# Optimization experiments

Measured on AMD Instinct MI355X. Metric: run time of the kernel, lower is better.

The kernel has to match this reference:

```python
import jax, jax.numpy as jnp
import numpy as np

B, N, M = 2, 8192, 8192
PEN_RATIO = 0.95
REG_W = 0.001
LOSS_W = 1.0
EPS_COS = 1e-8


def quat_to_rot(q):
    # q: [..., 4] in (x, y, z, w) order (legacy kornia convention), assumed normalized
    x, y, z, w = q[..., 0], q[..., 1], q[..., 2], q[..., 3]
    r0 = jnp.stack([1 - 2 * (y * y + z * z), 2 * (x * y - z * w), 2 * (x * z + y * w)], -1)
    r1 = jnp.stack([2 * (x * y + z * w), 1 - 2 * (x * x + z * z), 2 * (y * z - x * w)], -1)
    r2 = jnp.stack([2 * (x * z - y * w), 2 * (y * z + x * w), 1 - 2 * (x * x + y * y)], -1)
    return jnp.stack([r0, r1, r2], -2)


def span_cov(cp):
    # cp: [N,7] -> SPD cov [N,3,3]; eigenvalues are cumulative sums (e0, e0+e1, e0+e1+e2)
    e0 = cp[:, 0]
    e1 = e0 + cp[:, 1]
    e2 = e1 + cp[:, 2]
    eig = jnp.stack([e0, e1, e2], -1)  # [N,3]
    q = cp[:, 3:] / (jnp.linalg.norm(cp[:, 3:], axis=-1, keepdims=True) + 1e-9)
    E = quat_to_rot(q)  # [N,3,3]
    return jnp.einsum('nij,nj,nkj->nik', E, eig, E)


def setup_inputs() -> dict:
    key = jax.random.key(0)
    ks = jax.random.split(key, 8)
    return {
        'xyz_pred': jax.random.normal(ks[0], (B, N, 3), jnp.float32) * 10.0,
        'xyz_target': jax.random.normal(ks[1], (B, M, 3), jnp.float32) * 10.0,
        'cov_pred': jax.random.uniform(ks[2], (B, N, 7), jnp.float32),
        'cov_target': jax.random.uniform(ks[3], (B, M, 7), jnp.float32),
        'R_pred': jax.random.normal(ks[4], (B, 3, 3), jnp.float32),
        't_pred': jax.random.normal(ks[5], (B, 3), jnp.float32),
        'normal_pred': jax.random.normal(ks[6], (B, N, 3), jnp.float32),
        'normal_target': jax.random.normal(ks[7], (B, M, 3), jnp.float32),
    }


def reference(xyz_pred, xyz_target, cov_pred, cov_target, R_pred, t_pred, normal_pred, normal_target):
    def per_batch(xp, xt, cp, ct, R, nrm):
        covp = span_cov(cp)  # [N,3,3]
        covt = span_cov(ct)  # [M,3,3]
        # one-direction chamfer: squared NN distance + index (||p||^2+||t||^2-2 p.t)
        d2 = (xp * xp).sum(-1)[:, None] + (xt * xt).sum(-1)[None, :] - 2.0 * (xp @ xt.T)  # [N,M]
        diff = d2.min(axis=1)          # [N]
        idx = jnp.argmin(d2, axis=1)   # [N]
        xa = xt[idx]                   # associated target points
        cpa = covt[idx]                # associated target covariances
        dv = xp - xa
        # ROI mask via kth value: k = 1 + int(N*ratio) (1-indexed) -> sorted[int(N*ratio)]
        m = jnp.maximum(jnp.sort(diff)[int(N * PEN_RATIO)], 1.0)
        cm = (diff < m).astype(xp.dtype)
        nvalid = cm.sum()
        Rd = jax.lax.stop_gradient(R)
        sigma = covp + jnp.einsum('ij,njk,lk->nil', Rd, cpa, Rd)
        sigma_inv = jnp.linalg.inv(sigma)
        sq = jnp.einsum('ni,nij,nj->n', dv, sigma_inv, dv)  # Mahalanobis sq dist
        logdet = jnp.log(jnp.linalg.det(sigma))
        loss_b = (sq * cm).sum() / nvalid + REG_W * (0.5 * logdet * cm).sum() / nvalid
        # weighted SVD registration head (single ICP iter), all detached as in torch
        diff_na = xa - xp
        cossim = (nrm * diff_na).sum(-1) / jnp.maximum(
            jnp.linalg.norm(nrm, axis=-1) * jnp.linalg.norm(diff_na, axis=-1), EPS_COS)
        w = jax.lax.stop_gradient(jnp.abs(cossim) ** 2 * cm)
        src = jax.lax.stop_gradient(xp)
        tgt = jax.lax.stop_gradient(xa)
        wn = w / w.sum()
        sc = (wn[:, None] * src).sum(0)
        tc = (wn[:, None] * tgt).sum(0)
        H = jnp.einsum('n,ni,nj->ij', w, src - sc, tgt - tc)
        U, S, Vt = jnp.linalg.svd(H)
        V = Vt.T
        d = jnp.linalg.det(V @ U.T)
        Rres = V @ jnp.diag(jnp.stack([jnp.ones_like(d), jnp.ones_like(d), d])) @ U.T
        tres = tc - Rres @ sc
        return loss_b, Rres, tres

    losses, Rs, ts = jax.vmap(per_batch)(xyz_pred, xyz_target, cov_pred, cov_target, R_pred, normal_pred)
    return LOSS_W * losses.sum(), Rs, ts
```

## Files before the change

kernel.cpp:

```cpp
#include <hip/hip_runtime.h>
#include <math.h>

#define B_ 2
#define N_ 8192
#define M_ 8192
#define KSEL 7782
#define CH 128
#define CHS (M_ / CH)
#define PTS 1024
#define PPT 4

__device__ __forceinline__ unsigned ord_of(float f) {
  unsigned u = __float_as_uint(f);
  return (u & 0x80000000u) ? ~u : (u | 0x80000000u);
}
__device__ __forceinline__ float float_of_ord(unsigned o) {
  unsigned u = (o & 0x80000000u) ? (o ^ 0x80000000u) : ~o;
  return __uint_as_float(u);
}

__global__ __launch_bounds__(256) void init_kernel(
    unsigned long long* __restrict__ keys, const float* __restrict__ xt,
    float* __restrict__ tnorm) {
  const int gid = blockIdx.x * 256 + threadIdx.x;
  keys[gid] = 0xFFFFFFFFFFFFFFFFull;
  float tx = xt[gid * 3 + 0], ty = xt[gid * 3 + 1], tz = xt[gid * 3 + 2];
  tnorm[gid] = tx * tx + ty * ty + tz * tz;
}

__global__ __launch_bounds__(256, 8) void nn_kernel(
    const float* __restrict__ xp, const float* __restrict__ xt,
    const float* __restrict__ tnorm, unsigned long long* __restrict__ keys) {
  const int b = blockIdx.z;
  const int pblk = blockIdx.x;
  const int ch = blockIdx.y;

  __shared__ float4 tg[CHS];
  const float* __restrict__ xtb = xt + ((size_t)b * M_ + (size_t)ch * CHS) * 3;
  const float* __restrict__ twb = tnorm + (size_t)b * M_ + (size_t)ch * CHS;
  if (threadIdx.x < CHS) {
    const int j = threadIdx.x;
    tg[j] = make_float4(xtb[3 * j + 0], xtb[3 * j + 1], xtb[3 * j + 2],
                        twb[j]);
  }
  __syncthreads();

  const int i0 = pblk * PTS + threadIdx.x;
  float xm[PPT], ym[PPT], zm[PPT], nrm2[PPT], best[PPT];
  int bi[PPT];
#pragma unroll
  for (int k = 0; k < PPT; ++k) {
    const float* p = xp + ((size_t)b * N_ + i0 + k * 256) * 3;
    float x = p[0], y = p[1], z = p[2];
    nrm2[k] = x * x + y * y + z * z;
    xm[k] = -2.0f * x;
    ym[k] = -2.0f * y;
    zm[k] = -2.0f * z;
    best[k] = 3.4e38f;
    bi[k] = 0;
  }

#pragma unroll 2
  for (int j = 0; j < CHS; ++j) {
    float4 t = tg[j];
#pragma unroll
    for (int k = 0; k < PPT; ++k) {
      float d = fmaf(t.x, xm[k], fmaf(t.y, ym[k], fmaf(t.z, zm[k], t.w)));
      if (d < best[k]) { best[k] = d; bi[k] = j; }
    }
  }

  const int base = ch * CHS;
#pragma unroll
  for (int k = 0; k < PPT; ++k) {
    unsigned long long key =
        ((unsigned long long)ord_of(best[k] + nrm2[k]) << 32) |
        (unsigned)(base + bi[k]);
    atomicMin(&keys[(size_t)b * N_ + i0 + k * 256], key);
  }
}

__global__ __launch_bounds__(1024) void sel_kernel(
    const unsigned long long* __restrict__ keys, float* __restrict__ mout,
    double* __restrict__ acc) {
  __shared__ unsigned hist[256];
  __shared__ unsigned sel_digit, sel_rank;
  const int b = blockIdx.x;

  if (threadIdx.x < 32) acc[b * 32 + threadIdx.x] = 0.0;

  unsigned v[8];
#pragma unroll
  for (int t = 0; t < 8; ++t)
    v[t] = (unsigned)(keys[(size_t)b * N_ + threadIdx.x + t * 1024] >> 32);

  unsigned prefix = 0;
  unsigned rank = KSEL;

#pragma unroll
  for (int pass = 0; pass < 4; ++pass) {
    const int shift = 24 - pass * 8;
    const unsigned pmask = (pass == 0) ? 0u : (0xFFFFFFFFu << (shift + 8));

    if (threadIdx.x < 256) hist[threadIdx.x] = 0;
    __syncthreads();

#pragma unroll
    for (int t = 0; t < 8; ++t) {
      if ((v[t] & pmask) == prefix)
        atomicAdd(&hist[(v[t] >> shift) & 0xFFu], 1u);
    }
    __syncthreads();

    if (threadIdx.x < 64) {
      const int lane = threadIdx.x;
      unsigned h0 = hist[lane * 4 + 0], h1 = hist[lane * 4 + 1];
      unsigned h2 = hist[lane * 4 + 2], h3 = hist[lane * 4 + 3];
      unsigned c0 = h0, c1 = c0 + h1, c2 = c1 + h2, c3 = c2 + h3;
      unsigned s = c3;
#pragma unroll
      for (int off = 1; off < 64; off <<= 1) {
        unsigned t = __shfl_up(s, off);
        if (lane >= off) s += t;
      }
      unsigned excl = s - c3;
      unsigned r = rank;
      if (r >= excl && r < excl + c0) { sel_digit = lane * 4 + 0; sel_rank = r - excl; }
      if (r >= excl + c0 && r < excl + c1) { sel_digit = lane * 4 + 1; sel_rank = r - (excl + c0); }
      if (r >= excl + c1 && r < excl + c2) { sel_digit = lane * 4 + 2; sel_rank = r - (excl + c1); }
      if (r >= excl + c2 && r < excl + c3) { sel_digit = lane * 4 + 3; sel_rank = r - (excl + c2); }
    }
    __syncthreads();
    prefix |= (sel_digit << shift);
    rank = sel_rank;
    __syncthreads();
  }

  if (threadIdx.x == 0) {
    float f = float_of_ord(prefix);
    mout[b] = fmaxf(f, 1.0f);
  }
}

__device__ __forceinline__ void cov_from_params(const float* __restrict__ c,
                                                float C[3][3]) {
  float e0 = c[0];
  float e1 = e0 + c[1];
  float e2 = e1 + c[2];
  float qx = c[3], qy = c[4], qz = c[5], qw = c[6];
  float qn = sqrtf(qx * qx + qy * qy + qz * qz + qw * qw) + 1e-9f;
  float x = qx / qn, y = qy / qn, z = qz / qn, w = qw / qn;
  float E[3][3];
  E[0][0] = 1.0f - 2.0f * (y * y + z * z);
  E[0][1] = 2.0f * (x * y - z * w);
  E[0][2] = 2.0f * (x * z + y * w);
  E[1][0] = 2.0f * (x * y + z * w);
  E[1][1] = 1.0f - 2.0f * (x * x + z * z);
  E[1][2] = 2.0f * (y * z - x * w);
  E[2][0] = 2.0f * (x * z - y * w);
  E[2][1] = 2.0f * (y * z + x * w);
  E[2][2] = 1.0f - 2.0f * (x * x + y * y);
#pragma unroll
  for (int i = 0; i < 3; ++i)
#pragma unroll
    for (int k = 0; k < 3; ++k)
      C[i][k] = e0 * E[i][0] * E[k][0] + e1 * E[i][1] * E[k][1] +
                e2 * E[i][2] * E[k][2];
}

__global__ __launch_bounds__(256) void main_kernel(
    const float* __restrict__ xp, const float* __restrict__ xt,
    const float* __restrict__ cpp, const float* __restrict__ ctp,
    const float* __restrict__ Rp, const float* __restrict__ nrm,
    const unsigned long long* __restrict__ keys, const float* __restrict__ mout,
    double* __restrict__ acc) {
  const int b = blockIdx.y;
  const int i = blockIdx.x * 256 + threadIdx.x;

  float R[3][3];
#pragma unroll
  for (int r = 0; r < 3; ++r)
#pragma unroll
    for (int c = 0; c < 3; ++c) R[r][c] = Rp[b * 9 + r * 3 + c];
  const float m = mout[b];

  unsigned long long key = keys[(size_t)b * N_ + i];
  float d2 = float_of_ord((unsigned)(key >> 32));
  int id = (int)(key & 0xFFFFFFFFull);

  const float* p = xp + ((size_t)b * N_ + i) * 3;
  float px = p[0], py = p[1], pz = p[2];
  const float* a_ = xt + ((size_t)b * M_ + id) * 3;
  float ax = a_[0], ay = a_[1], az = a_[2];

  float cmv = (d2 < m) ? 1.0f : 0.0f;

  float Cp[3][3], Ct[3][3];
  cov_from_params(cpp + ((size_t)b * N_ + i) * 7, Cp);
  cov_from_params(ctp + ((size_t)b * M_ + id) * 7, Ct);

  float T[3][3], G[3][3];
#pragma unroll
  for (int r = 0; r < 3; ++r)
#pragma unroll
    for (int c = 0; c < 3; ++c)
      T[r][c] = R[r][0] * Ct[0][c] + R[r][1] * Ct[1][c] + R[r][2] * Ct[2][c];
#pragma unroll
  for (int r = 0; r < 3; ++r)
#pragma unroll
    for (int c = 0; c < 3; ++c)
      G[r][c] = Cp[r][c] +
                (T[r][0] * R[c][0] + T[r][1] * R[c][1] + T[r][2] * R[c][2]);

  float c00 = G[1][1] * G[2][2] - G[1][2] * G[2][1];
  float c01 = G[1][2] * G[2][0] - G[1][0] * G[2][2];
  float c02 = G[1][0] * G[2][1] - G[1][1] * G[2][0];
  float det = G[0][0] * c00 + G[0][1] * c01 + G[0][2] * c02;
  float rdet = 1.0f / det;
  float i00 = (G[1][1] * G[2][2] - G[1][2] * G[2][1]) * rdet;
  float i01 = (G[0][2] * G[2][1] - G[0][1] * G[2][2]) * rdet;
  float i02 = (G[0][1] * G[1][2] - G[0][2] * G[1][1]) * rdet;
  float i10 = (G[1][2] * G[2][0] - G[1][0] * G[2][2]) * rdet;
  float i11 = (G[0][0] * G[2][2] - G[0][2] * G[2][0]) * rdet;
  float i12 = (G[0][2] * G[1][0] - G[0][0] * G[1][2]) * rdet;
  float i20 = (G[1][0] * G[2][1] - G[1][1] * G[2][0]) * rdet;
  float i21 = (G[0][1] * G[2][0] - G[0][0] * G[2][1]) * rdet;
  float i22 = (G[0][0] * G[1][1] - G[0][1] * G[1][0]) * rdet;

  float dvx = px - ax, dvy = py - ay, dvz = pz - az;
  float t0 = i00 * dvx + i01 * dvy + i02 * dvz;
  float t1 = i10 * dvx + i11 * dvy + i12 * dvz;
  float t2 = i20 * dvx + i21 * dvy + i22 * dvz;
  float sq = dvx * t0 + dvy * t1 + dvz * t2;
  float logdet = logf(det);

  const float* nv = nrm + ((size_t)b * N_ + i) * 3;
  float nx = nv[0], ny = nv[1], nz = nv[2];
  float gx = ax - px, gy = ay - py, gz = az - pz;
  float dt = nx * gx + ny * gy + nz * gz;
  float den = fmaxf(sqrtf(nx * nx + ny * ny + nz * nz) *
                        sqrtf(gx * gx + gy * gy + gz * gz),
                    1e-8f);
  float cs = dt / den;
  float w = cs * cs * cmv;

  __shared__ double red[4][19];
  const int lane = threadIdx.x & 63, wv = threadIdx.x >> 6;

#define REDUCE_ONE(expr, kidx)                          \
  {                                                     \
    double v_ = (expr);                                 \
    v_ += __shfl_down(v_, 32);                          \
    v_ += __shfl_down(v_, 16);                          \
    v_ += __shfl_down(v_, 8);                           \
    v_ += __shfl_down(v_, 4);                           \
    v_ += __shfl_down(v_, 2);                           \
    v_ += __shfl_down(v_, 1);                           \
    if (lane == 0) red[wv][kidx] = v_;                  \
  }

  REDUCE_ONE((double)cmv, 0)
  REDUCE_ONE((double)sq * (double)cmv, 1)
  REDUCE_ONE((double)logdet * (double)cmv, 2)
  REDUCE_ONE((double)w, 3)
  REDUCE_ONE((double)w * px, 4)
  REDUCE_ONE((double)w * py, 5)
  REDUCE_ONE((double)w * pz, 6)
  REDUCE_ONE((double)w * ax, 7)
  REDUCE_ONE((double)w * ay, 8)
  REDUCE_ONE((double)w * az, 9)
  REDUCE_ONE((double)w * (double)px * (double)ax, 10)
  REDUCE_ONE((double)w * (double)px * (double)ay, 11)
  REDUCE_ONE((double)w * (double)px * (double)az, 12)
  REDUCE_ONE((double)w * (double)py * (double)ax, 13)
  REDUCE_ONE((double)w * (double)py * (double)ay, 14)
  REDUCE_ONE((double)w * (double)py * (double)az, 15)
  REDUCE_ONE((double)w * (double)pz * (double)ax, 16)
  REDUCE_ONE((double)w * (double)pz * (double)ay, 17)
  REDUCE_ONE((double)w * (double)pz * (double)az, 18)
#undef REDUCE_ONE

  __syncthreads();
  if (threadIdx.x < 19) {
    double s = red[0][threadIdx.x] + red[1][threadIdx.x] +
               red[2][threadIdx.x] + red[3][threadIdx.x];
    atomicAdd(&acc[b * 32 + threadIdx.x], s);
  }
}

__device__ float det3f(const float M[3][3]) {
  return M[0][0] * (M[1][1] * M[2][2] - M[1][2] * M[2][1]) -
         M[0][1] * (M[1][0] * M[2][2] - M[1][2] * M[2][0]) +
         M[0][2] * (M[1][0] * M[2][1] - M[1][1] * M[2][0]);
}

__device__ __forceinline__ void eigvec3f(const float A[3][3], float lam,
                                         float& vx, float& vy, float& vz) {
  float r00 = A[0][0] - lam, r01 = A[0][1], r02 = A[0][2];
  float r10 = A[0][1], r11 = A[1][1] - lam, r12 = A[1][2];
  float r20 = A[0][2], r21 = A[1][2], r22 = A[2][2] - lam;

  float ax = r01 * r12 - r02 * r11;
  float ay = r02 * r10 - r00 * r12;
  float az = r00 * r11 - r01 * r10;
  float bx = r01 * r22 - r02 * r21;
  float by = r02 * r20 - r00 * r22;
  float bz = r00 * r21 - r01 * r20;
  float cx = r11 * r22 - r12 * r21;
  float cy = r12 * r20 - r10 * r22;
  float cz = r10 * r21 - r11 * r20;

  float na = ax * ax + ay * ay + az * az;
  float nb = bx * bx + by * by + bz * bz;
  float nc = cx * cx + cy * cy + cz * cz;

  bool pickB = nb > na;
  float sx = pickB ? bx : ax, sy = pickB ? by : ay, sz = pickB ? bz : az;
  float sn = pickB ? nb : na;
  bool pickC = nc > sn;
  sx = pickC ? cx : sx; sy = pickC ? cy : sy; sz = pickC ? cz : sz;
  sn = pickC ? nc : sn;

  float inv = (sn > 0.0f) ? 1.0f / sqrtf(sn) : 0.0f;
  vx = sx * inv;
  vy = sy * inv;
  vz = sz * inv;
  if (inv == 0.0f) vx = 1.0f;
}

__device__ void kabschf(const float H[3][3], float R[3][3]) {
  float A[3][3];
#pragma unroll
  for (int i = 0; i < 3; ++i)
#pragma unroll
    for (int j = 0; j < 3; ++j)
      A[i][j] = H[0][i] * H[0][j] + H[1][i] * H[1][j] + H[2][i] * H[2][j];

  float lam0, lam1, lam2;
  float v0x, v0y, v0z, v1x, v1y, v1z, v2x, v2y, v2z;

  float mtr = (A[0][0] + A[1][1] + A[2][2]) / 3.0f;
  float K00 = A[0][0] - mtr, K11 = A[1][1] - mtr, K22 = A[2][2] - mtr;
  float a01 = A[0][1], a02 = A[0][2], a12 = A[1][2];
  float p2 = K00 * K00 + K11 * K11 + K22 * K22 +
             2.0f * (a01 * a01 + a02 * a02 + a12 * a12);
  float p = sqrtf(p2 / 6.0f);
  if (p < 1e-12f) {
    lam0 = lam1 = lam2 = mtr;
    v0x = 1.0f; v0y = 0.0f; v0z = 0.0f;
    v1x = 0.0f; v1y = 1.0f; v1z = 0.0f;
    v2x = 0.0f; v2y = 0.0f; v2z = 1.0f;
  } else {
    float detK = K00 * (K11 * K22 - a12 * a12) -
                 a01 * (a01 * K22 - a12 * a02) +
                 a02 * (a01 * a12 - K11 * a02);
    float rr = detK / (2.0f * p * p * p);
    rr = fminf(1.0f, fmaxf(-1.0f, rr));
    float phi = acosf(rr) / 3.0f;
    lam0 = mtr + 2.0f * p * cosf(phi);
    lam2 = mtr + 2.0f * p * cosf(phi + 2.0943951023931953f);
    lam1 = 3.0f * mtr - lam0 - lam2;

    eigvec3f(A, lam0, v0x, v0y, v0z);
    eigvec3f(A, lam1, v1x, v1y, v1z);
    float dp = v1x * v0x + v1y * v0y + v1z * v0z;
    v1x -= dp * v0x;
    v1y -= dp * v0y;
    v1z -= dp * v0z;
    float n1 = v1x * v1x + v1y * v1y + v1z * v1z;
    if (n1 > 1e-20f) {
      float inv = 1.0f / sqrtf(n1);
      v1x *= inv; v1y *= inv; v1z *= inv;
    } else {
      float fx = fabsf(v0x), fy = fabsf(v0y), fz = fabsf(v0z);
      bool xMin = (fx <= fy) && (fx <= fz);
      bool yMin = !xMin && (fy <= fz);
      float tx = xMin ? 1.0f : 0.0f;
      float ty = yMin ? 1.0f : 0.0f;
      float tz = (!xMin && !yMin) ? 1.0f : 0.0f;
      v1x = v0y * tz - v0z * ty;
      v1y = v0z * tx - v0x * tz;
      v1z = v0x * ty - v0y * tx;
      float inv = 1.0f / sqrtf(v1x * v1x + v1y * v1y + v1z * v1z);
      v1x *= inv; v1y *= inv; v1z *= inv;
    }
    v2x = v0y * v1z - v0z * v1y;
    v2y = v0z * v1x - v0x * v1z;
    v2z = v0x * v1y - v0y * v1x;
  }

  float Vs[3][3];
  Vs[0][0] = v0x; Vs[1][0] = v0y; Vs[2][0] = v0z;
  Vs[0][1] = v1x; Vs[1][1] = v1y; Vs[2][1] = v1z;
  Vs[0][2] = v2x; Vs[1][2] = v2y; Vs[2][2] = v2z;

  float sg0 = sqrtf(fmaxf(lam0, 0.0f));
  float sg1 = sqrtf(fmaxf(lam1, 0.0f));
  float sg2 = sqrtf(fmaxf(lam2, 0.0f));

  float U[3][3];
  {
    float sg[3] = {sg0, sg1, sg2};
#pragma unroll
    for (int c = 0; c < 3; ++c) {
      float ux = H[0][0] * Vs[0][c] + H[0][1] * Vs[1][c] + H[0][2] * Vs[2][c];
      float uy = H[1][0] * Vs[0][c] + H[1][1] * Vs[1][c] + H[1][2] * Vs[2][c];
      float uz = H[2][0] * Vs[0][c] + H[2][1] * Vs[1][c] + H[2][2] * Vs[2][c];
      float inv = (sg[c] > 1e-6f * sg0 + 1e-30f) ? 1.0f / sg[c] : 0.0f;
      U[0][c] = ux * inv;
      U[1][c] = uy * inv;
      U[2][c] = uz * inv;
    }
  }
  if (sg2 <= 1e-6f * sg0 + 1e-30f) {
    U[0][2] = U[1][0] * U[2][1] - U[2][0] * U[1][1];
    U[1][2] = U[2][0] * U[0][1] - U[0][0] * U[2][1];
    U[2][2] = U[0][0] * U[1][1] - U[1][0] * U[0][1];
  }
  float d = det3f(U) * det3f(Vs);
#pragma unroll
  for (int i = 0; i < 3; ++i)
#pragma unroll
    for (int j = 0; j < 3; ++j)
      R[i][j] = Vs[i][0] * U[j][0] + Vs[i][1] * U[j][1] + d * Vs[i][2] * U[j][2];
}

__global__ __launch_bounds__(64) void finalize_kernel(
    const double* __restrict__ acc, float* __restrict__ out) {
  __shared__ double lossb[B_];
  const int b = threadIdx.x;
  if (b < B_) {
    const double* a = acc + b * 32;
    double cnt = a[0], ssq = a[1], sld = a[2], W = a[3];
    double loss = ssq / cnt + 0.001 * 0.5 * sld / cnt;
    lossb[b] = loss;
    double Ss[3] = {a[4], a[5], a[6]}, St[3] = {a[7], a[8], a[9]};
    double sc[3], tc[3];
#pragma unroll
    for (int c = 0; c < 3; ++c) { sc[c] = Ss[c] / W; tc[c] = St[c] / W; }
    double H[3][3];
    double hmax = 1e-30;
#pragma unroll
    for (int r = 0; r < 3; ++r)
#pragma unroll
      for (int c = 0; c < 3; ++c) {
        H[r][c] = a[10 + r * 3 + c] - Ss[r] * St[c] / W;
        double ab = fabs(H[r][c]);
        if (ab > hmax) hmax = ab;
      }
    float Hf[3][3];
    double rinv = 1.0 / hmax;
#pragma unroll
    for (int r = 0; r < 3; ++r)
#pragma unroll
      for (int c = 0; c < 3; ++c) Hf[r][c] = (float)(H[r][c] * rinv);
    float Rf[3][3];
    kabschf(Hf, Rf);
#pragma unroll
    for (int r = 0; r < 3; ++r)
#pragma unroll
      for (int c = 0; c < 3; ++c)
        out[1 + b * 9 + r * 3 + c] = Rf[r][c];
#pragma unroll
    for (int r = 0; r < 3; ++r) {
      double t = tc[r] - ((double)Rf[r][0] * sc[0] + (double)Rf[r][1] * sc[1] +
                          (double)Rf[r][2] * sc[2]);
      out[1 + B_ * 9 + b * 3 + r] = (float)t;
    }
  }
  __syncthreads();
  if (threadIdx.x == 0) out[0] = (float)(lossb[0] + lossb[1]);
}

extern "C" void kernel_launch(void* const* d_in, const int* in_sizes, int n_in,
                              void* d_out, int out_size, void* d_ws,
                              size_t ws_size, hipStream_t stream) {
  const float* xyz_pred = (const float*)d_in[0];
  const float* xyz_target = (const float*)d_in[1];
  const float* cov_pred = (const float*)d_in[2];
  const float* cov_target = (const float*)d_in[3];
  const float* R_pred = (const float*)d_in[4];
  const float* normal_pred = (const float*)d_in[6];
  float* out = (float*)d_out;

  char* ws = (char*)d_ws;
  double* acc = (double*)ws;
  unsigned long long* keys = (unsigned long long*)(ws + 512);
  float* mout = (float*)(ws + 512 + (size_t)B_ * N_ * 8);
  float* tnorm = (float*)(ws + 1024 + (size_t)B_ * N_ * 8);

  hipLaunchKernelGGL(init_kernel, dim3(B_ * M_ / 256), dim3(256), 0, stream,
                     keys, xyz_target, tnorm);
  hipLaunchKernelGGL(nn_kernel, dim3(N_ / PTS, CH, B_), dim3(256), 0, stream,
                     xyz_pred, xyz_target, tnorm, keys);
  hipLaunchKernelGGL(sel_kernel, dim3(B_), dim3(1024), 0, stream, keys, mout,
                     acc);
  hipLaunchKernelGGL(main_kernel, dim3(N_ / 256, B_), dim3(256), 0, stream,
                     xyz_pred, xyz_target, cov_pred, cov_target, R_pred,
                     normal_pred, keys, mout, acc);
  hipLaunchKernelGGL(finalize_kernel, dim3(1), dim3(64), 0, stream, acc, out);
}
```

Baseline: 48.05 us.

## Fuse radix select, main loss and finalize into one tail kernel

Merges the selection, per-point loss and finalize kernels into a single tail kernel. Each block redundantly recomputes the batch's radix-select threshold, and the last block to finish (found through an atomic counter) runs the Kabsch finalize. Accumulator zeroing moves into the init kernel. This removes two kernel launches and their inter-kernel gaps. In exchange, all 32 blocks per batch repeat the 8192-key histogram passes with only 256 threads each.

```diff
diff --git a/kernel.cpp b/kernel.cpp
--- a/kernel.cpp
+++ b/kernel.cpp
@@ -21,11 +21,14 @@
 
 __global__ __launch_bounds__(256) void init_kernel(
     unsigned long long* __restrict__ keys, const float* __restrict__ xt,
-    float* __restrict__ tnorm) {
+    float* __restrict__ tnorm, double* __restrict__ acc,
+    unsigned* __restrict__ done) {
   const int gid = blockIdx.x * 256 + threadIdx.x;
   keys[gid] = 0xFFFFFFFFFFFFFFFFull;
   float tx = xt[gid * 3 + 0], ty = xt[gid * 3 + 1], tz = xt[gid * 3 + 2];
   tnorm[gid] = tx * tx + ty * ty + tz * tz;
+  if (gid < B_ * 32) acc[gid] = 0.0;
+  if (gid == 0) *done = 0u;
 }
 
 __global__ __launch_bounds__(256, 8) void nn_kernel(
@@ -77,68 +80,6 @@
         ((unsigned long long)ord_of(best[k] + nrm2[k]) << 32) |
         (unsigned)(base + bi[k]);
     atomicMin(&keys[(size_t)b * N_ + i0 + k * 256], key);
-  }
-}
-
-__global__ __launch_bounds__(1024) void sel_kernel(
-    const unsigned long long* __restrict__ keys, float* __restrict__ mout,
-    double* __restrict__ acc) {
-  __shared__ unsigned hist[256];
-  __shared__ unsigned sel_digit, sel_rank;
-  const int b = blockIdx.x;
-
-  if (threadIdx.x < 32) acc[b * 32 + threadIdx.x] = 0.0;
-
-  unsigned v[8];
-#pragma unroll
-  for (int t = 0; t < 8; ++t)
-    v[t] = (unsigned)(keys[(size_t)b * N_ + threadIdx.x + t * 1024] >> 32);
-
-  unsigned prefix = 0;
-  unsigned rank = KSEL;
-
-#pragma unroll
-  for (int pass = 0; pass < 4; ++pass) {
-    const int shift = 24 - pass * 8;
-    const unsigned pmask = (pass == 0) ? 0u : (0xFFFFFFFFu << (shift + 8));
-
-    if (threadIdx.x < 256) hist[threadIdx.x] = 0;
-    __syncthreads();
-
-#pragma unroll
-    for (int t = 0; t < 8; ++t) {
-      if ((v[t] & pmask) == prefix)
-        atomicAdd(&hist[(v[t] >> shift) & 0xFFu], 1u);
-    }
-    __syncthreads();
-
-    if (threadIdx.x < 64) {
-      const int lane = threadIdx.x;
-      unsigned h0 = hist[lane * 4 + 0], h1 = hist[lane * 4 + 1];
-      unsigned h2 = hist[lane * 4 + 2], h3 = hist[lane * 4 + 3];
-      unsigned c0 = h0, c1 = c0 + h1, c2 = c1 + h2, c3 = c2 + h3;
-      unsigned s = c3;
-#pragma unroll
-      for (int off = 1; off < 64; off <<= 1) {
-        unsigned t = __shfl_up(s, off);
-        if (lane >= off) s += t;
-      }
-      unsigned excl = s - c3;
-      unsigned r = rank;
-      if (r >= excl && r < excl + c0) { sel_digit = lane * 4 + 0; sel_rank = r - excl; }
-      if (r >= excl + c0 && r < excl + c1) { sel_digit = lane * 4 + 1; sel_rank = r - (excl + c0); }
-      if (r >= excl + c1 && r < excl + c2) { sel_digit = lane * 4 + 2; sel_rank = r - (excl + c1); }
-      if (r >= excl + c2 && r < excl + c3) { sel_digit = lane * 4 + 3; sel_rank = r - (excl + c2); }
-    }
-    __syncthreads();
-    prefix |= (sel_digit << shift);
-    rank = sel_rank;
-    __syncthreads();
-  }
-
-  if (threadIdx.x == 0) {
-    float f = float_of_ord(prefix);
-    mout[b] = fmaxf(f, 1.0f);
   }
 }
 
@@ -166,126 +107,6 @@
     for (int k = 0; k < 3; ++k)
       C[i][k] = e0 * E[i][0] * E[k][0] + e1 * E[i][1] * E[k][1] +
                 e2 * E[i][2] * E[k][2];
-}
-
-__global__ __launch_bounds__(256) void main_kernel(
-    const float* __restrict__ xp, const float* __restrict__ xt,
-    const float* __restrict__ cpp, const float* __restrict__ ctp,
-    const float* __restrict__ Rp, const float* __restrict__ nrm,
-    const unsigned long long* __restrict__ keys, const float* __restrict__ mout,
-    double* __restrict__ acc) {
-  const int b = blockIdx.y;
-  const int i = blockIdx.x * 256 + threadIdx.x;
-
-  float R[3][3];
-#pragma unroll
-  for (int r = 0; r < 3; ++r)
-#pragma unroll
-    for (int c = 0; c < 3; ++c) R[r][c] = Rp[b * 9 + r * 3 + c];
-  const float m = mout[b];
-
-  unsigned long long key = keys[(size_t)b * N_ + i];
-  float d2 = float_of_ord((unsigned)(key >> 32));
-  int id = (int)(key & 0xFFFFFFFFull);
-
-  const float* p = xp + ((size_t)b * N_ + i) * 3;
-  float px = p[0], py = p[1], pz = p[2];
-  const float* a_ = xt + ((size_t)b * M_ + id) * 3;
-  float ax = a_[0], ay = a_[1], az = a_[2];
-
-  float cmv = (d2 < m) ? 1.0f : 0.0f;
-
-  float Cp[3][3], Ct[3][3];
-  cov_from_params(cpp + ((size_t)b * N_ + i) * 7, Cp);
-  cov_from_params(ctp + ((size_t)b * M_ + id) * 7, Ct);
-
-  float T[3][3], G[3][3];
-#pragma unroll
-  for (int r = 0; r < 3; ++r)
-#pragma unroll
-    for (int c = 0; c < 3; ++c)
-      T[r][c] = R[r][0] * Ct[0][c] + R[r][1] * Ct[1][c] + R[r][2] * Ct[2][c];
-#pragma unroll
-  for (int r = 0; r < 3; ++r)
-#pragma unroll
-    for (int c = 0; c < 3; ++c)
-      G[r][c] = Cp[r][c] +
-                (T[r][0] * R[c][0] + T[r][1] * R[c][1] + T[r][2] * R[c][2]);
-
-  float c00 = G[1][1] * G[2][2] - G[1][2] * G[2][1];
-  float c01 = G[1][2] * G[2][0] - G[1][0] * G[2][2];
-  float c02 = G[1][0] * G[2][1] - G[1][1] * G[2][0];
-  float det = G[0][0] * c00 + G[0][1] * c01 + G[0][2] * c02;
-  float rdet = 1.0f / det;
-  float i00 = (G[1][1] * G[2][2] - G[1][2] * G[2][1]) * rdet;
-  float i01 = (G[0][2] * G[2][1] - G[0][1] * G[2][2]) * rdet;
-  float i02 = (G[0][1] * G[1][2] - G[0][2] * G[1][1]) * rdet;
-  float i10 = (G[1][2] * G[2][0] - G[1][0] * G[2][2]) * rdet;
-  float i11 = (G[0][0] * G[2][2] - G[0][2] * G[2][0]) * rdet;
-  float i12 = (G[0][2] * G[1][0] - G[0][0] * G[1][2]) * rdet;
-  float i20 = (G[1][0] * G[2][1] - G[1][1] * G[2][0]) * rdet;
-  float i21 = (G[0][1] * G[2][0] - G[0][0] * G[2][1]) * rdet;
-  float i22 = (G[0][0] * G[1][1] - G[0][1] * G[1][0]) * rdet;
-
-  float dvx = px - ax, dvy = py - ay, dvz = pz - az;
-  float t0 = i00 * dvx + i01 * dvy + i02 * dvz;
-  float t1 = i10 * dvx + i11 * dvy + i12 * dvz;
-  float t2 = i20 * dvx + i21 * dvy + i22 * dvz;
-  float sq = dvx * t0 + dvy * t1 + dvz * t2;
-  float logdet = logf(det);
-
-  const float* nv = nrm + ((size_t)b * N_ + i) * 3;
-  float nx = nv[0], ny = nv[1], nz = nv[2];
-  float gx = ax - px, gy = ay - py, gz = az - pz;
-  float dt = nx * gx + ny * gy + nz * gz;
-  float den = fmaxf(sqrtf(nx * nx + ny * ny + nz * nz) *
-                        sqrtf(gx * gx + gy * gy + gz * gz),
-                    1e-8f);
-  float cs = dt / den;
-  float w = cs * cs * cmv;
-
-  __shared__ double red[4][19];
-  const int lane = threadIdx.x & 63, wv = threadIdx.x >> 6;
-
-#define REDUCE_ONE(expr, kidx)                          \
-  {                                                     \
-    double v_ = (expr);                                 \
-    v_ += __shfl_down(v_, 32);                          \
-    v_ += __shfl_down(v_, 16);                          \
-    v_ += __shfl_down(v_, 8);                           \
-    v_ += __shfl_down(v_, 4);                           \
-    v_ += __shfl_down(v_, 2);                           \
-    v_ += __shfl_down(v_, 1);                           \
-    if (lane == 0) red[wv][kidx] = v_;                  \
-  }
-
-  REDUCE_ONE((double)cmv, 0)
-  REDUCE_ONE((double)sq * (double)cmv, 1)
-  REDUCE_ONE((double)logdet * (double)cmv, 2)
-  REDUCE_ONE((double)w, 3)
-  REDUCE_ONE((double)w * px, 4)
-  REDUCE_ONE((double)w * py, 5)
-  REDUCE_ONE((double)w * pz, 6)
-  REDUCE_ONE((double)w * ax, 7)
-  REDUCE_ONE((double)w * ay, 8)
-  REDUCE_ONE((double)w * az, 9)
-  REDUCE_ONE((double)w * (double)px * (double)ax, 10)
-  REDUCE_ONE((double)w * (double)px * (double)ay, 11)
-  REDUCE_ONE((double)w * (double)px * (double)az, 12)
-  REDUCE_ONE((double)w * (double)py * (double)ax, 13)
-  REDUCE_ONE((double)w * (double)py * (double)ay, 14)
-  REDUCE_ONE((double)w * (double)py * (double)az, 15)
-  REDUCE_ONE((double)w * (double)pz * (double)ax, 16)
-  REDUCE_ONE((double)w * (double)pz * (double)ay, 17)
-  REDUCE_ONE((double)w * (double)pz * (double)az, 18)
-#undef REDUCE_ONE
-
-  __syncthreads();
-  if (threadIdx.x < 19) {
-    double s = red[0][threadIdx.x] + red[1][threadIdx.x] +
-               red[2][threadIdx.x] + red[3][threadIdx.x];
-    atomicAdd(&acc[b * 32 + threadIdx.x], s);
-  }
 }
 
 __device__ float det3f(const float M[3][3]) {
@@ -425,15 +246,192 @@
       R[i][j] = Vs[i][0] * U[j][0] + Vs[i][1] * U[j][1] + d * Vs[i][2] * U[j][2];
 }
 
-__global__ __launch_bounds__(64) void finalize_kernel(
-    const double* __restrict__ acc, float* __restrict__ out) {
+__global__ __launch_bounds__(256) void tail_kernel(
+    const float* __restrict__ xp, const float* __restrict__ xt,
+    const float* __restrict__ cpp, const float* __restrict__ ctp,
+    const float* __restrict__ Rp, const float* __restrict__ nrm,
+    const unsigned long long* __restrict__ keys, double* __restrict__ acc,
+    unsigned* __restrict__ done, float* __restrict__ out) {
+  const int b = blockIdx.y;
+  const unsigned* __restrict__ keyhi =
+      (const unsigned*)(keys + (size_t)b * N_) + 1;
+
+  __shared__ unsigned hist[256];
+  __shared__ unsigned sel_digit, sel_rank;
+  __shared__ float m_sh;
+  {
+    unsigned prefix = 0, rank = KSEL;
+#pragma unroll
+    for (int pass = 0; pass < 4; ++pass) {
+      const int shift = 24 - pass * 8;
+      const unsigned pmask = (pass == 0) ? 0u : (0xFFFFFFFFu << (shift + 8));
+      hist[threadIdx.x] = 0;
+      __syncthreads();
+#pragma unroll 4
+      for (int t = 0; t < 32; ++t) {
+        unsigned v = keyhi[2 * (threadIdx.x + t * 256)];
+        if ((v & pmask) == prefix)
+          atomicAdd(&hist[(v >> shift) & 0xFFu], 1u);
+      }
+      __syncthreads();
+      if (threadIdx.x < 64) {
+        const int lane = threadIdx.x;
+        unsigned h0 = hist[lane * 4 + 0], h1 = hist[lane * 4 + 1];
+        unsigned h2 = hist[lane * 4 + 2], h3 = hist[lane * 4 + 3];
+        unsigned c0 = h0, c1 = c0 + h1, c2 = c1 + h2, c3 = c2 + h3;
+        unsigned s = c3;
+#pragma unroll
+        for (int off = 1; off < 64; off <<= 1) {
+          unsigned t = __shfl_up(s, off);
+          if (lane >= off) s += t;
+        }
+        unsigned excl = s - c3;
+        unsigned r = rank;
+        if (r >= excl && r < excl + c0) { sel_digit = lane * 4 + 0; sel_rank = r - excl; }
+        if (r >= excl + c0 && r < excl + c1) { sel_digit = lane * 4 + 1; sel_rank = r - (excl + c0); }
+        if (r >= excl + c1 && r < excl + c2) { sel_digit = lane * 4 + 2; sel_rank = r - (excl + c1); }
+        if (r >= excl + c2 && r < excl + c3) { sel_digit = lane * 4 + 3; sel_rank = r - (excl + c2); }
+      }
+      __syncthreads();
+      prefix |= (sel_digit << shift);
+      rank = sel_rank;
+      __syncthreads();
+    }
+    if (threadIdx.x == 0) m_sh = fmaxf(float_of_ord(prefix), 1.0f);
+    __syncthreads();
+  }
+  const float m = m_sh;
+
+  const int i = blockIdx.x * 256 + threadIdx.x;
+
+  float R[3][3];
+#pragma unroll
+  for (int r = 0; r < 3; ++r)
+#pragma unroll
+    for (int c = 0; c < 3; ++c) R[r][c] = Rp[b * 9 + r * 3 + c];
+
+  unsigned long long key = keys[(size_t)b * N_ + i];
+  float d2 = float_of_ord((unsigned)(key >> 32));
+  int id = (int)(key & 0xFFFFFFFFull);
+
+  const float* p = xp + ((size_t)b * N_ + i) * 3;
+  float px = p[0], py = p[1], pz = p[2];
+  const float* a_ = xt + ((size_t)b * M_ + id) * 3;
+  float ax = a_[0], ay = a_[1], az = a_[2];
+
+  float cmv = (d2 < m) ? 1.0f : 0.0f;
+
+  float Cp[3][3], Ct[3][3];
+  cov_from_params(cpp + ((size_t)b * N_ + i) * 7, Cp);
+  cov_from_params(ctp + ((size_t)b * M_ + id) * 7, Ct);
+
+  float T[3][3], G[3][3];
+#pragma unroll
+  for (int r = 0; r < 3; ++r)
+#pragma unroll
+    for (int c = 0; c < 3; ++c)
+      T[r][c] = R[r][0] * Ct[0][c] + R[r][1] * Ct[1][c] + R[r][2] * Ct[2][c];
+#pragma unroll
+  for (int r = 0; r < 3; ++r)
+#pragma unroll
+    for (int c = 0; c < 3; ++c)
+      G[r][c] = Cp[r][c] +
+                (T[r][0] * R[c][0] + T[r][1] * R[c][1] + T[r][2] * R[c][2]);
+
+  float c00 = G[1][1] * G[2][2] - G[1][2] * G[2][1];
+  float c01 = G[1][2] * G[2][0] - G[1][0] * G[2][2];
+  float c02 = G[1][0] * G[2][1] - G[1][1] * G[2][0];
+  float det = G[0][0] * c00 + G[0][1] * c01 + G[0][2] * c02;
+  float rdet = 1.0f / det;
+  float i00 = (G[1][1] * G[2][2] - G[1][2] * G[2][1]) * rdet;
+  float i01 = (G[0][2] * G[2][1] - G[0][1] * G[2][2]) * rdet;
+  float i02 = (G[0][1] * G[1][2] - G[0][2] * G[1][1]) * rdet;
+  float i10 = (G[1][2] * G[2][0] - G[1][0] * G[2][2]) * rdet;
+  float i11 = (G[0][0] * G[2][2] - G[0][2] * G[2][0]) * rdet;
+  float i12 = (G[0][2] * G[1][0] - G[0][0] * G[1][2]) * rdet;
+  float i20 = (G[1][0] * G[2][1] - G[1][1] * G[2][0]) * rdet;
+  float i21 = (G[0][1] * G[2][0] - G[0][0] * G[2][1]) * rdet;
+  float i22 = (G[0][0] * G[1][1] - G[0][1] * G[1][0]) * rdet;
+
+  float dvx = px - ax, dvy = py - ay, dvz = pz - az;
+  float t0 = i00 * dvx + i01 * dvy + i02 * dvz;
+  float t1 = i10 * dvx + i11 * dvy + i12 * dvz;
+  float t2 = i20 * dvx + i21 * dvy + i22 * dvz;
+  float sq = dvx * t0 + dvy * t1 + dvz * t2;
+  float logdet = logf(det);
+
+  const float* nv = nrm + ((size_t)b * N_ + i) * 3;
+  float nx = nv[0], ny = nv[1], nz = nv[2];
+  float gx = ax - px, gy = ay - py, gz = az - pz;
+  float dt = nx * gx + ny * gy + nz * gz;
+  float den = fmaxf(sqrtf(nx * nx + ny * ny + nz * nz) *
+                        sqrtf(gx * gx + gy * gy + gz * gz),
+                    1e-8f);
+  float cs = dt / den;
+  float w = cs * cs * cmv;
+
+  __shared__ double red[4][19];
+  const int lane = threadIdx.x & 63, wv = threadIdx.x >> 6;
+
+#define REDUCE_ONE(expr, kidx)                          \
+  {                                                     \
+    double v_ = (expr);                                 \
+    v_ += __shfl_down(v_, 32);                          \
+    v_ += __shfl_down(v_, 16);                          \
+    v_ += __shfl_down(v_, 8);                           \
+    v_ += __shfl_down(v_, 4);                           \
+    v_ += __shfl_down(v_, 2);                           \
+    v_ += __shfl_down(v_, 1);                           \
+    if (lane == 0) red[wv][kidx] = v_;                  \
+  }
+
+  REDUCE_ONE((double)cmv, 0)
+  REDUCE_ONE((double)sq * (double)cmv, 1)
+  REDUCE_ONE((double)logdet * (double)cmv, 2)
+  REDUCE_ONE((double)w, 3)
+  REDUCE_ONE((double)w * px, 4)
+  REDUCE_ONE((double)w * py, 5)
+  REDUCE_ONE((double)w * pz, 6)
+  REDUCE_ONE((double)w * ax, 7)
+  REDUCE_ONE((double)w * ay, 8)
+  REDUCE_ONE((double)w * az, 9)
+  REDUCE_ONE((double)w * (double)px * (double)ax, 10)
+  REDUCE_ONE((double)w * (double)px * (double)ay, 11)
+  REDUCE_ONE((double)w * (double)px * (double)az, 12)
+  REDUCE_ONE((double)w * (double)py * (double)ax, 13)
+  REDUCE_ONE((double)w * (double)py * (double)ay, 14)
+  REDUCE_ONE((double)w * (double)py * (double)az, 15)
+  REDUCE_ONE((double)w * (double)pz * (double)ax, 16)
+  REDUCE_ONE((double)w * (double)pz * (double)ay, 17)
+  REDUCE_ONE((double)w * (double)pz * (double)az, 18)
+#undef REDUCE_ONE
+
+  __syncthreads();
+  if (threadIdx.x < 19) {
+    double s = red[0][threadIdx.x] + red[1][threadIdx.x] +
+               red[2][threadIdx.x] + red[3][threadIdx.x];
+    atomicAdd(&acc[b * 32 + threadIdx.x], s);
+  }
+
+  __shared__ bool amLast;
+  __threadfence();
+  if (threadIdx.x == 0) {
+    unsigned old = atomicAdd(done, 1u);
+    amLast = (old == 32u * B_ - 1u);
+  }
+  __syncthreads();
+  if (!amLast) return;
+  __threadfence();
+
   __shared__ double lossb[B_];
-  const int b = threadIdx.x;
-  if (b < B_) {
-    const double* a = acc + b * 32;
+  const int fb = threadIdx.x;
+  if (fb < B_) {
+    double a[19];
+#pragma unroll
+    for (int k = 0; k < 19; ++k)
+      a[k] = atomicAdd(&acc[fb * 32 + k], 0.0);
     double cnt = a[0], ssq = a[1], sld = a[2], W = a[3];
-    double loss = ssq / cnt + 0.001 * 0.5 * sld / cnt;
-    lossb[b] = loss;
+    lossb[fb] = ssq / cnt + 0.001 * 0.5 * sld / cnt;
     double Ss[3] = {a[4], a[5], a[6]}, St[3] = {a[7], a[8], a[9]};
     double sc[3], tc[3];
 #pragma unroll
@@ -460,12 +458,12 @@
     for (int r = 0; r < 3; ++r)
 #pragma unroll
       for (int c = 0; c < 3; ++c)
-        out[1 + b * 9 + r * 3 + c] = Rf[r][c];
+        out[1 + fb * 9 + r * 3 + c] = Rf[r][c];
 #pragma unroll
     for (int r = 0; r < 3; ++r) {
       double t = tc[r] - ((double)Rf[r][0] * sc[0] + (double)Rf[r][1] * sc[1] +
                           (double)Rf[r][2] * sc[2]);
-      out[1 + B_ * 9 + b * 3 + r] = (float)t;
+      out[1 + B_ * 9 + fb * 3 + r] = (float)t;
     }
   }
   __syncthreads();
@@ -485,18 +483,15 @@
 
   char* ws = (char*)d_ws;
   double* acc = (double*)ws;
-  unsigned long long* keys = (unsigned long long*)(ws + 512);
-  float* mout = (float*)(ws + 512 + (size_t)B_ * N_ * 8);
+  unsigned* done = (unsigned*)(ws + 512);
+  unsigned long long* keys = (unsigned long long*)(ws + 1024);
   float* tnorm = (float*)(ws + 1024 + (size_t)B_ * N_ * 8);
 
   hipLaunchKernelGGL(init_kernel, dim3(B_ * M_ / 256), dim3(256), 0, stream,
-                     keys, xyz_target, tnorm);
+                     keys, xyz_target, tnorm, acc, done);
   hipLaunchKernelGGL(nn_kernel, dim3(N_ / PTS, CH, B_), dim3(256), 0, stream,
                      xyz_pred, xyz_target, tnorm, keys);
-  hipLaunchKernelGGL(sel_kernel, dim3(B_), dim3(1024), 0, stream, keys, mout,
-                     acc);
-  hipLaunchKernelGGL(main_kernel, dim3(N_ / 256, B_), dim3(256), 0, stream,
+  hipLaunchKernelGGL(tail_kernel, dim3(32, B_), dim3(256), 0, stream,
                      xyz_pred, xyz_target, cov_pred, cov_target, R_pred,
-                     normal_pred, keys, mout, acc);
-  hipLaunchKernelGGL(finalize_kernel, dim3(1), dim3(64), 0, stream, acc, out);
-}
+                     normal_pred, keys, acc, done, out);
+}
```

After: 63.56 us. +32.3%, slower.
